# Optimization experiments

Measured on AMD Instinct MI355X. Metric: run time of the kernel, lower is better.

Reference implementation:

```python
import jax, jax.numpy as jnp
import numpy as np

# dims: batch, seq, embed, hidden (=4*embed), experts, top-k
B, T, D, H, E, K = 2, 4096, 1024, 4096, 8, 2


def setup_inputs() -> dict:
    key = jax.random.key(0)
    ks = jax.random.split(key, 5)
    scale = 0.02
    x = jax.random.normal(ks[0], (B, T, D), dtype=jnp.float32)
    Wr = jax.random.normal(ks[1], (D, E), dtype=jnp.float32) * scale   # router weight (no bias)
    W1 = jax.random.normal(ks[2], (E, D, H), dtype=jnp.float32) * scale  # stacked expert fc1
    b1 = jnp.zeros((E, H), dtype=jnp.float32)
    W2 = jax.random.normal(ks[3], (E, H, D), dtype=jnp.float32) * scale  # stacked expert fc2
    b2 = jnp.zeros((E, D), dtype=jnp.float32)
    return {"x": x, "Wr": Wr, "W1": W1, "b1": b1, "W2": W2, "b2": b2}


def reference(x, Wr, W1, b1, W2, b2):
    # ---- Router (eval mode: no noise) ----
    logits = jnp.einsum('btd,de->bte', x, Wr)                 # [B,T,E]
    probs = jax.nn.softmax(logits, axis=-1)
    w, idx = jax.lax.top_k(probs, K)                          # [B,T,K]
    w = w / jnp.sum(w, axis=-1, keepdims=True)                # renormalize top-k weights
    # dispatch tensor: scatter normalized weights back to expert slots
    dispatch = jnp.sum(jax.nn.one_hot(idx, E, dtype=x.dtype) * w[..., None], axis=-2)  # [B,T,E]

    # ---- Experts: each expert FFN runs densely over ALL tokens (as in source), then masked-accumulate ----
    h = jax.nn.gelu(jnp.einsum('btd,edh->ebth', x, W1) + b1[:, None, None, :], approximate=False)  # [E,B,T,H]
    y = jnp.einsum('ebth,ehd->ebtd', h, W2) + b2[:, None, None, :]                                 # [E,B,T,D]
    out = jnp.einsum('ebtd,bte->btd', y, dispatch)            # weighted accumulate over experts
    return out
```

## Files before the change

kernel.cpp:

```cpp
#include <hip/hip_runtime.h>
#include <hip/hip_bf16.h>
#include <math.h>

#define NTOK  8192
#define DD    1024
#define HH    4096
#define EE    8
#define NSLOT (NTOK*2)

typedef __attribute__((ext_vector_type(8))) short bf16x8;
typedef __attribute__((ext_vector_type(4))) float f32x4;

static __device__ __forceinline__ float gelu_exact(float v) {
    return 0.5f * v * (1.0f + erff(v * 0.70710678118654752f));
}

__global__ __launch_bounds__(256) void cvt_x_kernel(const float* __restrict__ x,
                                                    __hip_bfloat16* __restrict__ xb) {
    int i = (blockIdx.x * 256 + threadIdx.x) * 4;
    float4 v = *(const float4*)(x + i);
    __hip_bfloat162 lo = __float22bfloat162_rn(make_float2(v.x, v.y));
    __hip_bfloat162 hi = __float22bfloat162_rn(make_float2(v.z, v.w));
    *(__hip_bfloat162*)(xb + i)     = lo;
    *(__hip_bfloat162*)(xb + i + 2) = hi;
}

__global__ __launch_bounds__(256) void cvt_w_t_kernel(const float* __restrict__ src,
                                                      __hip_bfloat16* __restrict__ dst,
                                                      int R, int C) {
    __shared__ float tile[32][33];
    int e = blockIdx.z;
    size_t base = (size_t)e * R * C;
    int c0 = blockIdx.x * 32, r0 = blockIdx.y * 32;
    int tx = threadIdx.x, ty = threadIdx.y;
    #pragma unroll
    for (int q = 0; q < 4; ++q)
        tile[ty + q * 8][tx] = src[base + (size_t)(r0 + ty + q * 8) * C + (c0 + tx)];
    __syncthreads();
    #pragma unroll
    for (int q = 0; q < 4; ++q)
        dst[base + (size_t)(c0 + ty + q * 8) * R + (r0 + tx)] =
            __float2bfloat16(tile[tx][ty + q * 8]);
}

__global__ __launch_bounds__(256) void router_kernel(const float* __restrict__ x,
                                                     const float* __restrict__ Wr,
                                                     int* __restrict__ topk_idx,
                                                     float* __restrict__ topk_w,
                                                     int* __restrict__ counts) {
    __shared__ float wr[DD * 9];
    for (int i = threadIdx.x; i < DD * EE; i += 256) {
        int d = i >> 3, e = i & 7;
        wr[d * 9 + e] = Wr[i];
    }
    __syncthreads();
    int wave = threadIdx.x >> 6, lane = threadIdx.x & 63;
    int t = blockIdx.x * 4 + wave;
    const float* xr = x + (size_t)t * DD;
    float acc[EE] = {};
    for (int j = 0; j < DD / 64; ++j) {
        float v = xr[j * 64 + lane];
        int d = j * 64 + lane;
        #pragma unroll
        for (int e = 0; e < EE; ++e) acc[e] += v * wr[d * 9 + e];
    }
    #pragma unroll
    for (int off = 32; off > 0; off >>= 1)
        #pragma unroll
        for (int e = 0; e < EE; ++e) acc[e] += __shfl_xor(acc[e], off);
    if (lane == 0) {
        int e1 = 0;
        #pragma unroll
        for (int e = 1; e < EE; ++e) if (acc[e] > acc[e1]) e1 = e;
        int e2 = (e1 == 0) ? 1 : 0;
        #pragma unroll
        for (int e = 0; e < EE; ++e)
            if (e != e1 && e != e2 && acc[e] > acc[e2]) e2 = e;
        float w1 = 1.0f / (1.0f + expf(acc[e2] - acc[e1]));
        topk_idx[t * 2]     = e1;
        topk_idx[t * 2 + 1] = e2;
        topk_w[t * 2]       = w1;
        topk_w[t * 2 + 1]   = 1.0f - w1;
        atomicAdd(&counts[e1], 1);
        atomicAdd(&counts[e2], 1);
    }
}

__global__ void prefix_kernel(const int* __restrict__ counts,
                              int* __restrict__ offsets, int* __restrict__ cursors) {
    if (threadIdx.x == 0 && blockIdx.x == 0) {
        int s = 0;
        for (int e = 0; e < EE; ++e) { offsets[e] = s; cursors[e] = s; s += counts[e]; }
        offsets[EE] = s;
    }
}

__global__ __launch_bounds__(256) void scatter_kernel(const int* __restrict__ topk_idx,
                                                      const float* __restrict__ topk_w,
                                                      int* __restrict__ cursors,
                                                      int* __restrict__ btok,
                                                      float* __restrict__ bw) {
    int t = blockIdx.x * 256 + threadIdx.x;
    if (t >= NTOK) return;
    #pragma unroll
    for (int k = 0; k < 2; ++k) {
        int e = topk_idx[t * 2 + k];
        int p = atomicAdd(&cursors[e], 1);
        btok[p] = t;
        bw[p]   = topk_w[t * 2 + k];
    }
}

__global__ __launch_bounds__(256) void fc1_kernel(
    const __hip_bfloat16* __restrict__ xb, const __hip_bfloat16* __restrict__ w1t,
    const float* __restrict__ b1, const int* __restrict__ offsets,
    const int* __restrict__ btok, __hip_bfloat16* __restrict__ hbuf,
    int h0, int Cchunk) {
    int e = blockIdx.z;
    int seg0 = offsets[e];
    int cnt  = offsets[e + 1] - seg0;
    int m0 = blockIdx.y * 128;
    if (m0 >= cnt) return;
    int n0 = h0 + blockIdx.x * 128;

    __shared__ __hip_bfloat16 As[128 * 40];
    __shared__ __hip_bfloat16 Bs[128 * 40];

    int tid = threadIdx.x;
    int r = tid >> 2, cq = (tid & 3) * 8;
    int arow0 = m0 + r, arow1 = m0 + r + 64;
    int tok0 = btok[seg0 + (arow0 < cnt ? arow0 : 0)];
    int tok1 = btok[seg0 + (arow1 < cnt ? arow1 : 0)];
    const __hip_bfloat16* ap0 = xb + (size_t)tok0 * DD + cq;
    const __hip_bfloat16* ap1 = xb + (size_t)tok1 * DD + cq;
    const __hip_bfloat16* bp0 = w1t + ((size_t)e * HH + n0 + r) * DD + cq;
    const __hip_bfloat16* bp1 = w1t + ((size_t)e * HH + n0 + r + 64) * DD + cq;

    int wv = tid >> 6, lane = tid & 63;
    int wr_ = wv >> 1, wc = wv & 1;
    int q = lane >> 4, lc = lane & 15;

    f32x4 acc[4][4] = {};

    for (int k0 = 0; k0 < DD; k0 += 32) {
        uint4 av0 = *(const uint4*)(ap0 + k0);
        uint4 av1 = *(const uint4*)(ap1 + k0);
        uint4 bv0 = *(const uint4*)(bp0 + k0);
        uint4 bv1 = *(const uint4*)(bp1 + k0);
        __syncthreads();
        *(uint4*)(As + r * 40 + cq)        = av0;
        *(uint4*)(As + (r + 64) * 40 + cq) = av1;
        *(uint4*)(Bs + r * 40 + cq)        = bv0;
        *(uint4*)(Bs + (r + 64) * 40 + cq) = bv1;
        __syncthreads();
        bf16x8 af[4], bg[4];
        #pragma unroll
        for (int i = 0; i < 4; ++i)
            af[i] = *(const bf16x8*)(As + (wr_ * 64 + i * 16 + lc) * 40 + q * 8);
        #pragma unroll
        for (int j = 0; j < 4; ++j)
            bg[j] = *(const bf16x8*)(Bs + (wc * 64 + j * 16 + lc) * 40 + q * 8);
        #pragma unroll
        for (int i = 0; i < 4; ++i)
            #pragma unroll
            for (int j = 0; j < 4; ++j)
                acc[i][j] = __builtin_amdgcn_mfma_f32_16x16x32_bf16(af[i], bg[j], acc[i][j], 0, 0, 0);
    }

    #pragma unroll
    for (int i = 0; i < 4; ++i) {
        #pragma unroll
        for (int j = 0; j < 4; ++j) {
            int col = n0 + wc * 64 + j * 16 + lc;
            float bias = b1[e * HH + col];
            #pragma unroll
            for (int rg = 0; rg < 4; ++rg) {
                int ml = wr_ * 64 + i * 16 + q * 4 + rg;
                if (m0 + ml < cnt) {
                    float v = acc[i][j][rg] + bias;
                    hbuf[(size_t)(seg0 + m0 + ml) * Cchunk + (col - h0)] =
                        __float2bfloat16(gelu_exact(v));
                }
            }
        }
    }
}

__global__ __launch_bounds__(256) void fc2_kernel(
    const __hip_bfloat16* __restrict__ hbuf, const __hip_bfloat16* __restrict__ w2t,
    const float* __restrict__ b2, const int* __restrict__ offsets,
    const int* __restrict__ btok, const float* __restrict__ bw,
    float* __restrict__ out, int h0, int Cchunk) {
    int e = blockIdx.z;
    int seg0 = offsets[e];
    int cnt  = offsets[e + 1] - seg0;
    int m0 = blockIdx.y * 128;
    if (m0 >= cnt) return;
    int n0 = blockIdx.x * 128;

    __shared__ __hip_bfloat16 As[128 * 40];
    __shared__ __hip_bfloat16 Bs[128 * 40];

    int tid = threadIdx.x;
    int r = tid >> 2, cq = (tid & 3) * 8;
    int arow0 = m0 + r, arow1 = m0 + r + 64;
    int slot0 = seg0 + (arow0 < cnt ? arow0 : 0);
    int slot1 = seg0 + (arow1 < cnt ? arow1 : 0);
    const __hip_bfloat16* ap0 = hbuf + (size_t)slot0 * Cchunk + cq;
    const __hip_bfloat16* ap1 = hbuf + (size_t)slot1 * Cchunk + cq;
    const __hip_bfloat16* bp0 = w2t + ((size_t)e * DD + n0 + r) * HH + h0 + cq;
    const __hip_bfloat16* bp1 = w2t + ((size_t)e * DD + n0 + r + 64) * HH + h0 + cq;

    int wv = tid >> 6, lane = tid & 63;
    int wr_ = wv >> 1, wc = wv & 1;
    int q = lane >> 4, lc = lane & 15;

    f32x4 acc[4][4] = {};

    for (int k0 = 0; k0 < Cchunk; k0 += 32) {
        uint4 av0 = *(const uint4*)(ap0 + k0);
        uint4 av1 = *(const uint4*)(ap1 + k0);
        uint4 bv0 = *(const uint4*)(bp0 + k0);
        uint4 bv1 = *(const uint4*)(bp1 + k0);
        __syncthreads();
        *(uint4*)(As + r * 40 + cq)        = av0;
        *(uint4*)(As + (r + 64) * 40 + cq) = av1;
        *(uint4*)(Bs + r * 40 + cq)        = bv0;
        *(uint4*)(Bs + (r + 64) * 40 + cq) = bv1;
        __syncthreads();
        bf16x8 af[4], bg[4];
        #pragma unroll
        for (int i = 0; i < 4; ++i)
            af[i] = *(const bf16x8*)(As + (wr_ * 64 + i * 16 + lc) * 40 + q * 8);
        #pragma unroll
        for (int j = 0; j < 4; ++j)
            bg[j] = *(const bf16x8*)(Bs + (wc * 64 + j * 16 + lc) * 40 + q * 8);
        #pragma unroll
        for (int i = 0; i < 4; ++i)
            #pragma unroll
            for (int j = 0; j < 4; ++j)
                acc[i][j] = __builtin_amdgcn_mfma_f32_16x16x32_bf16(af[i], bg[j], acc[i][j], 0, 0, 0);
    }

    #pragma unroll
    for (int i = 0; i < 4; ++i) {
        #pragma unroll
        for (int j = 0; j < 4; ++j) {
            int col = n0 + wc * 64 + j * 16 + lc;
            float bias = b2[e * DD + col];
            #pragma unroll
            for (int rg = 0; rg < 4; ++rg) {
                int ml = wr_ * 64 + i * 16 + q * 4 + rg;
                if (m0 + ml < cnt) {
                    int s = seg0 + m0 + ml;
                    int t = btok[s];
                    float w = bw[s];
                    float add = w * acc[i][j][rg];
                    if (h0 == 0) add += w * bias;
                    atomicAdd(out + (size_t)t * DD + col, add);
                }
            }
        }
    }
}

static inline size_t alignup(size_t v, size_t a) { return (v + a - 1) & ~(a - 1); }

extern "C" void kernel_launch(void* const* d_in, const int* in_sizes, int n_in,
                              void* d_out, int out_size, void* d_ws, size_t ws_size,
                              hipStream_t stream) {
    const float* x  = (const float*)d_in[0];
    const float* Wr = (const float*)d_in[1];
    const float* W1 = (const float*)d_in[2];
    const float* b1 = (const float*)d_in[3];
    const float* W2 = (const float*)d_in[4];
    const float* b2 = (const float*)d_in[5];
    float* out = (float*)d_out;

    char* p = (char*)d_ws;
    size_t off = 0;
    int* counts  = (int*)(p + off); off += 64;
    int* offsets = (int*)(p + off); off += 64;
    int* cursors = (int*)(p + off); off += 64;
    off = alignup(off, 256);
    int*   topk_idx = (int*)(p + off);   off += (size_t)NTOK * 2 * 4;
    float* topk_w   = (float*)(p + off); off += (size_t)NTOK * 2 * 4;
    int*   btok     = (int*)(p + off);   off += (size_t)NSLOT * 4;
    float* bwt      = (float*)(p + off); off += (size_t)NSLOT * 4;
    off = alignup(off, 256);
    __hip_bfloat16* xb  = (__hip_bfloat16*)(p + off); off += (size_t)NTOK * DD * 2;
    __hip_bfloat16* w1t = (__hip_bfloat16*)(p + off); off += (size_t)EE * DD * HH * 2;
    __hip_bfloat16* w2t = (__hip_bfloat16*)(p + off); off += (size_t)EE * DD * HH * 2;
    off = alignup(off, 256);
    __hip_bfloat16* hbuf = (__hip_bfloat16*)(p + off);
    size_t rem = (ws_size > off) ? (ws_size - off) : 0;
    int C = HH;
    while (C > 128 && (size_t)NSLOT * C * 2 > rem) C >>= 1;

    hipMemsetAsync(d_out, 0, (size_t)NTOK * DD * 4, stream);
    hipMemsetAsync(counts, 0, 192, stream);

    cvt_x_kernel<<<NTOK * DD / 1024, 256, 0, stream>>>(x, xb);
    cvt_w_t_kernel<<<dim3(HH / 32, DD / 32, EE), dim3(32, 8), 0, stream>>>(W1, w1t, DD, HH);
    cvt_w_t_kernel<<<dim3(DD / 32, HH / 32, EE), dim3(32, 8), 0, stream>>>(W2, w2t, HH, DD);
    router_kernel<<<NTOK / 4, 256, 0, stream>>>(x, Wr, topk_idx, topk_w, counts);
    prefix_kernel<<<1, 64, 0, stream>>>(counts, offsets, cursors);
    scatter_kernel<<<NTOK / 256, 256, 0, stream>>>(topk_idx, topk_w, cursors, btok, bwt);

    for (int h0 = 0; h0 < HH; h0 += C) {
        fc1_kernel<<<dim3(C / 128, NTOK / 128, EE), 256, 0, stream>>>(
            xb, w1t, b1, offsets, btok, hbuf, h0, C);
        fc2_kernel<<<dim3(DD / 128, NTOK / 128, EE), 256, 0, stream>>>(
            hbuf, w2t, b2, offsets, btok, bwt, out, h0, C);
    }
}
```

Before: 1.241 ms.

## Use direct global-to-LDS loads in GEMMs and replace atomic scatter with combine pass

Result: faster. 1.139 ms (-8.2%).

```diff
diff --git a/kernel.cpp b/kernel.cpp
--- a/kernel.cpp
+++ b/kernel.cpp
@@ -13,6 +13,12 @@
 
 static __device__ __forceinline__ float gelu_exact(float v) {
     return 0.5f * v * (1.0f + erff(v * 0.70710678118654752f));
+}
+
+static __device__ __forceinline__ void gload16(const void* g, void* l) {
+    __builtin_amdgcn_global_load_lds(
+        (const __attribute__((address_space(1))) void*)g,
+        (__attribute__((address_space(3))) void*)l, 16, 0, 0);
 }
 
 __global__ __launch_bounds__(256) void cvt_x_kernel(const float* __restrict__ x,
@@ -96,10 +102,9 @@
 }
 
 __global__ __launch_bounds__(256) void scatter_kernel(const int* __restrict__ topk_idx,
-                                                      const float* __restrict__ topk_w,
                                                       int* __restrict__ cursors,
                                                       int* __restrict__ btok,
-                                                      float* __restrict__ bw) {
+                                                      int* __restrict__ slot_of) {
     int t = blockIdx.x * 256 + threadIdx.x;
     if (t >= NTOK) return;
     #pragma unroll
@@ -107,13 +112,13 @@
         int e = topk_idx[t * 2 + k];
         int p = atomicAdd(&cursors[e], 1);
         btok[p] = t;
-        bw[p]   = topk_w[t * 2 + k];
+        slot_of[t * 2 + k] = p;
     }
 }
 
 __global__ __launch_bounds__(256) void fc1_kernel(
     const __hip_bfloat16* __restrict__ xb, const __hip_bfloat16* __restrict__ w1t,
-    const float* __restrict__ b1, const int* __restrict__ offsets,
+    const float* __restrict__ b1g, const int* __restrict__ offsets,
     const int* __restrict__ btok, __hip_bfloat16* __restrict__ hbuf,
     int h0, int Cchunk) {
     int e = blockIdx.z;
@@ -123,48 +128,52 @@
     if (m0 >= cnt) return;
     int n0 = h0 + blockIdx.x * 128;
 
-    __shared__ __hip_bfloat16 As[128 * 40];
-    __shared__ __hip_bfloat16 Bs[128 * 40];
+    __shared__ __align__(16) __hip_bfloat16 As[128 * 32];
+    __shared__ __align__(16) __hip_bfloat16 Bs[128 * 32];
 
     int tid = threadIdx.x;
-    int r = tid >> 2, cq = (tid & 3) * 8;
-    int arow0 = m0 + r, arow1 = m0 + r + 64;
-    int tok0 = btok[seg0 + (arow0 < cnt ? arow0 : 0)];
-    int tok1 = btok[seg0 + (arow1 < cnt ? arow1 : 0)];
-    const __hip_bfloat16* ap0 = xb + (size_t)tok0 * DD + cq;
-    const __hip_bfloat16* ap1 = xb + (size_t)tok1 * DD + cq;
-    const __hip_bfloat16* bp0 = w1t + ((size_t)e * HH + n0 + r) * DD + cq;
-    const __hip_bfloat16* bp1 = w1t + ((size_t)e * HH + n0 + r + 64) * DD + cq;
-
     int wv = tid >> 6, lane = tid & 63;
+    int lr  = lane >> 2;
+    int lcq = lane & 3;
+
+    int ra0 = wv * 32 + lr;
+    int ra1 = ra0 + 16;
+    int ga0 = m0 + ra0, ga1 = m0 + ra1;
+    int tok0 = btok[seg0 + (ga0 < cnt ? ga0 : 0)];
+    int tok1 = btok[seg0 + (ga1 < cnt ? ga1 : 0)];
+    const __hip_bfloat16* a0 = xb + (size_t)tok0 * DD + lcq * 8;
+    const __hip_bfloat16* a1 = xb + (size_t)tok1 * DD + lcq * 8;
+    const __hip_bfloat16* b0 = w1t + ((size_t)e * HH + n0 + ra0) * DD + lcq * 8;
+    const __hip_bfloat16* b1p = w1t + ((size_t)e * HH + n0 + ra1) * DD + lcq * 8;
+    __hip_bfloat16* lA0 = As + (wv * 32) * 32;
+    __hip_bfloat16* lA1 = As + (wv * 32 + 16) * 32;
+    __hip_bfloat16* lB0 = Bs + (wv * 32) * 32;
+    __hip_bfloat16* lB1 = Bs + (wv * 32 + 16) * 32;
+
     int wr_ = wv >> 1, wc = wv & 1;
     int q = lane >> 4, lc = lane & 15;
 
     f32x4 acc[4][4] = {};
 
     for (int k0 = 0; k0 < DD; k0 += 32) {
-        uint4 av0 = *(const uint4*)(ap0 + k0);
-        uint4 av1 = *(const uint4*)(ap1 + k0);
-        uint4 bv0 = *(const uint4*)(bp0 + k0);
-        uint4 bv1 = *(const uint4*)(bp1 + k0);
-        __syncthreads();
-        *(uint4*)(As + r * 40 + cq)        = av0;
-        *(uint4*)(As + (r + 64) * 40 + cq) = av1;
-        *(uint4*)(Bs + r * 40 + cq)        = bv0;
-        *(uint4*)(Bs + (r + 64) * 40 + cq) = bv1;
+        gload16(a0 + k0, lA0);
+        gload16(a1 + k0, lA1);
+        gload16(b0 + k0, lB0);
+        gload16(b1p + k0, lB1);
         __syncthreads();
         bf16x8 af[4], bg[4];
         #pragma unroll
         for (int i = 0; i < 4; ++i)
-            af[i] = *(const bf16x8*)(As + (wr_ * 64 + i * 16 + lc) * 40 + q * 8);
+            af[i] = *(const bf16x8*)(As + (wr_ * 64 + i * 16 + lc) * 32 + q * 8);
         #pragma unroll
         for (int j = 0; j < 4; ++j)
-            bg[j] = *(const bf16x8*)(Bs + (wc * 64 + j * 16 + lc) * 40 + q * 8);
+            bg[j] = *(const bf16x8*)(Bs + (wc * 64 + j * 16 + lc) * 32 + q * 8);
         #pragma unroll
         for (int i = 0; i < 4; ++i)
             #pragma unroll
             for (int j = 0; j < 4; ++j)
                 acc[i][j] = __builtin_amdgcn_mfma_f32_16x16x32_bf16(af[i], bg[j], acc[i][j], 0, 0, 0);
+        __syncthreads();
     }
 
     #pragma unroll
@@ -172,7 +181,7 @@
         #pragma unroll
         for (int j = 0; j < 4; ++j) {
             int col = n0 + wc * 64 + j * 16 + lc;
-            float bias = b1[e * HH + col];
+            float bias = b1g[e * HH + col];
             #pragma unroll
             for (int rg = 0; rg < 4; ++rg) {
                 int ml = wr_ * 64 + i * 16 + q * 4 + rg;
@@ -188,9 +197,8 @@
 
 __global__ __launch_bounds__(256) void fc2_kernel(
     const __hip_bfloat16* __restrict__ hbuf, const __hip_bfloat16* __restrict__ w2t,
-    const float* __restrict__ b2, const int* __restrict__ offsets,
-    const int* __restrict__ btok, const float* __restrict__ bw,
-    float* __restrict__ out, int h0, int Cchunk) {
+    const int* __restrict__ offsets, float* __restrict__ ybuf,
+    int h0, int Cchunk) {
     int e = blockIdx.z;
     int seg0 = offsets[e];
     int cnt  = offsets[e + 1] - seg0;
@@ -198,48 +206,52 @@
     if (m0 >= cnt) return;
     int n0 = blockIdx.x * 128;
 
-    __shared__ __hip_bfloat16 As[128 * 40];
-    __shared__ __hip_bfloat16 Bs[128 * 40];
+    __shared__ __align__(16) __hip_bfloat16 As[128 * 32];
+    __shared__ __align__(16) __hip_bfloat16 Bs[128 * 32];
 
     int tid = threadIdx.x;
-    int r = tid >> 2, cq = (tid & 3) * 8;
-    int arow0 = m0 + r, arow1 = m0 + r + 64;
-    int slot0 = seg0 + (arow0 < cnt ? arow0 : 0);
-    int slot1 = seg0 + (arow1 < cnt ? arow1 : 0);
-    const __hip_bfloat16* ap0 = hbuf + (size_t)slot0 * Cchunk + cq;
-    const __hip_bfloat16* ap1 = hbuf + (size_t)slot1 * Cchunk + cq;
-    const __hip_bfloat16* bp0 = w2t + ((size_t)e * DD + n0 + r) * HH + h0 + cq;
-    const __hip_bfloat16* bp1 = w2t + ((size_t)e * DD + n0 + r + 64) * HH + h0 + cq;
-
     int wv = tid >> 6, lane = tid & 63;
+    int lr  = lane >> 2;
+    int lcq = lane & 3;
+
+    int ra0 = wv * 32 + lr;
+    int ra1 = ra0 + 16;
+    int ga0 = m0 + ra0, ga1 = m0 + ra1;
+    int slot0 = seg0 + (ga0 < cnt ? ga0 : 0);
+    int slot1 = seg0 + (ga1 < cnt ? ga1 : 0);
+    const __hip_bfloat16* a0 = hbuf + (size_t)slot0 * Cchunk + lcq * 8;
+    const __hip_bfloat16* a1 = hbuf + (size_t)slot1 * Cchunk + lcq * 8;
+    const __hip_bfloat16* b0 = w2t + ((size_t)e * DD + n0 + ra0) * HH + h0 + lcq * 8;
+    const __hip_bfloat16* b1p = w2t + ((size_t)e * DD + n0 + ra1) * HH + h0 + lcq * 8;
+    __hip_bfloat16* lA0 = As + (wv * 32) * 32;
+    __hip_bfloat16* lA1 = As + (wv * 32 + 16) * 32;
+    __hip_bfloat16* lB0 = Bs + (wv * 32) * 32;
+    __hip_bfloat16* lB1 = Bs + (wv * 32 + 16) * 32;
+
     int wr_ = wv >> 1, wc = wv & 1;
     int q = lane >> 4, lc = lane & 15;
 
     f32x4 acc[4][4] = {};
 
     for (int k0 = 0; k0 < Cchunk; k0 += 32) {
-        uint4 av0 = *(const uint4*)(ap0 + k0);
-        uint4 av1 = *(const uint4*)(ap1 + k0);
-        uint4 bv0 = *(const uint4*)(bp0 + k0);
-        uint4 bv1 = *(const uint4*)(bp1 + k0);
-        __syncthreads();
-        *(uint4*)(As + r * 40 + cq)        = av0;
-        *(uint4*)(As + (r + 64) * 40 + cq) = av1;
-        *(uint4*)(Bs + r * 40 + cq)        = bv0;
-        *(uint4*)(Bs + (r + 64) * 40 + cq) = bv1;
+        gload16(a0 + k0, lA0);
+        gload16(a1 + k0, lA1);
+        gload16(b0 + k0, lB0);
+        gload16(b1p + k0, lB1);
         __syncthreads();
         bf16x8 af[4], bg[4];
         #pragma unroll
         for (int i = 0; i < 4; ++i)
-            af[i] = *(const bf16x8*)(As + (wr_ * 64 + i * 16 + lc) * 40 + q * 8);
+            af[i] = *(const bf16x8*)(As + (wr_ * 64 + i * 16 + lc) * 32 + q * 8);
         #pragma unroll
         for (int j = 0; j < 4; ++j)
-            bg[j] = *(const bf16x8*)(Bs + (wc * 64 + j * 16 + lc) * 40 + q * 8);
+            bg[j] = *(const bf16x8*)(Bs + (wc * 64 + j * 16 + lc) * 32 + q * 8);
         #pragma unroll
         for (int i = 0; i < 4; ++i)
             #pragma unroll
             for (int j = 0; j < 4; ++j)
                 acc[i][j] = __builtin_amdgcn_mfma_f32_16x16x32_bf16(af[i], bg[j], acc[i][j], 0, 0, 0);
+        __syncthreads();
     }
 
     #pragma unroll
@@ -247,21 +259,39 @@
         #pragma unroll
         for (int j = 0; j < 4; ++j) {
             int col = n0 + wc * 64 + j * 16 + lc;
-            float bias = b2[e * DD + col];
             #pragma unroll
             for (int rg = 0; rg < 4; ++rg) {
                 int ml = wr_ * 64 + i * 16 + q * 4 + rg;
                 if (m0 + ml < cnt) {
-                    int s = seg0 + m0 + ml;
-                    int t = btok[s];
-                    float w = bw[s];
-                    float add = w * acc[i][j][rg];
-                    if (h0 == 0) add += w * bias;
-                    atomicAdd(out + (size_t)t * DD + col, add);
+                    size_t yi = (size_t)(seg0 + m0 + ml) * DD + col;
+                    float v = acc[i][j][rg];
+                    ybuf[yi] = (h0 == 0) ? v : (ybuf[yi] + v);
                 }
             }
         }
     }
+}
+
+__global__ __launch_bounds__(256) void combine_kernel(
+    const float* __restrict__ ybuf, const float* __restrict__ b2,
+    const int* __restrict__ topk_idx, const float* __restrict__ topk_w,
+    const int* __restrict__ slot_of, float* __restrict__ out) {
+    int idx = blockIdx.x * 256 + threadIdx.x;
+    int t  = idx >> 8;
+    int d4 = (idx & 255) * 4;
+    int e0 = topk_idx[t * 2], e1 = topk_idx[t * 2 + 1];
+    float w0 = topk_w[t * 2], w1 = topk_w[t * 2 + 1];
+    int s0 = slot_of[t * 2], s1 = slot_of[t * 2 + 1];
+    float4 y0 = *(const float4*)(ybuf + (size_t)s0 * DD + d4);
+    float4 y1 = *(const float4*)(ybuf + (size_t)s1 * DD + d4);
+    float4 c0 = *(const float4*)(b2 + e0 * DD + d4);
+    float4 c1 = *(const float4*)(b2 + e1 * DD + d4);
+    float4 o;
+    o.x = w0 * (y0.x + c0.x) + w1 * (y1.x + c1.x);
+    o.y = w0 * (y0.y + c0.y) + w1 * (y1.y + c1.y);
+    o.z = w0 * (y0.z + c0.z) + w1 * (y1.z + c1.z);
+    o.w = w0 * (y0.w + c0.w) + w1 * (y1.w + c1.w);
+    *(float4*)(out + (size_t)t * DD + d4) = o;
 }
 
 static inline size_t alignup(size_t v, size_t a) { return (v + a - 1) & ~(a - 1); }
@@ -286,18 +316,18 @@
     int*   topk_idx = (int*)(p + off);   off += (size_t)NTOK * 2 * 4;
     float* topk_w   = (float*)(p + off); off += (size_t)NTOK * 2 * 4;
     int*   btok     = (int*)(p + off);   off += (size_t)NSLOT * 4;
-    float* bwt      = (float*)(p + off); off += (size_t)NSLOT * 4;
+    int*   slot_of  = (int*)(p + off);   off += (size_t)NTOK * 2 * 4;
     off = alignup(off, 256);
     __hip_bfloat16* xb  = (__hip_bfloat16*)(p + off); off += (size_t)NTOK * DD * 2;
     __hip_bfloat16* w1t = (__hip_bfloat16*)(p + off); off += (size_t)EE * DD * HH * 2;
     __hip_bfloat16* w2t = (__hip_bfloat16*)(p + off); off += (size_t)EE * DD * HH * 2;
+    float* ybuf = (float*)(p + off);                  off += (size_t)NSLOT * DD * 4;
     off = alignup(off, 256);
     __hip_bfloat16* hbuf = (__hip_bfloat16*)(p + off);
     size_t rem = (ws_size > off) ? (ws_size - off) : 0;
     int C = HH;
     while (C > 128 && (size_t)NSLOT * C * 2 > rem) C >>= 1;
 
-    hipMemsetAsync(d_out, 0, (size_t)NTOK * DD * 4, stream);
     hipMemsetAsync(counts, 0, 192, stream);
 
     cvt_x_kernel<<<NTOK * DD / 1024, 256, 0, stream>>>(x, xb);
@@ -305,12 +335,14 @@
     cvt_w_t_kernel<<<dim3(DD / 32, HH / 32, EE), dim3(32, 8), 0, stream>>>(W2, w2t, HH, DD);
     router_kernel<<<NTOK / 4, 256, 0, stream>>>(x, Wr, topk_idx, topk_w, counts);
     prefix_kernel<<<1, 64, 0, stream>>>(counts, offsets, cursors);
-    scatter_kernel<<<NTOK / 256, 256, 0, stream>>>(topk_idx, topk_w, cursors, btok, bwt);
+    scatter_kernel<<<NTOK / 256, 256, 0, stream>>>(topk_idx, cursors, btok, slot_of);
 
     for (int h0 = 0; h0 < HH; h0 += C) {
         fc1_kernel<<<dim3(C / 128, NTOK / 128, EE), 256, 0, stream>>>(
             xb, w1t, b1, offsets, btok, hbuf, h0, C);
         fc2_kernel<<<dim3(DD / 128, NTOK / 128, EE), 256, 0, stream>>>(
-            hbuf, w2t, b2, offsets, btok, bwt, out, h0, C);
-    }
-}
+            hbuf, w2t, offsets, ybuf, h0, C);
+    }
+    combine_kernel<<<NTOK * DD / 4 / 256, 256, 0, stream>>>(
+        ybuf, b2, topk_idx, topk_w, slot_of, out);
+}
```
